# Kernel optimization log

Measured on AMD Instinct MI355X. Metric: run time of the kernel, lower is better.

The kernel has to match this reference:

```python
import jax, jax.numpy as jnp
import numpy as np
from jax import lax

B, L, H = 2, 1024, 1024
D = 2048          # intermediate_size
N = 16            # ssm state size
K = 4             # conv kernel
R = 64            # time_step_rank


def setup_inputs() -> dict:
    key = jax.random.key(0)
    ks = jax.random.split(key, 10)
    def nrm(k, shape, scale=0.02):
        return jax.random.normal(k, shape, dtype=jnp.float32) * scale
    A = jnp.arange(1, N + 1, dtype=jnp.float32)[None, :] * jnp.ones((D, 1), jnp.float32)
    return {
        "hidden_states": jax.random.normal(ks[0], (B, L, H), dtype=jnp.float32),
        "W_in":  nrm(ks[1], (2 * D, H)),
        "conv_w": nrm(ks[2], (D, 1, K), 0.1),
        "conv_b": nrm(ks[3], (D,), 0.1),
        "W_x":   nrm(ks[4], (R + 2 * N, D)),
        "W_dt":  nrm(ks[5], (D, R), 0.1),
        "b_dt":  jnp.full((D,), -4.6, jnp.float32),  # softplus(-4.6) ~ 0.01 dt init
        "A_log": jnp.log(A),
        "D_param": jnp.ones((D,), jnp.float32),
        "W_out": nrm(ks[6], (H, D)),
    }


def _mamba_forward(hidden_states, W_in, conv_w, conv_b, W_x, W_dt, b_dt, A_log, D_param, W_out):
    silu = jax.nn.silu
    # in_proj -> [B, L, 2D], chunk into x and gate
    proj = jnp.einsum("blh,eh->ble", hidden_states, W_in)
    x, gate = jnp.split(proj, 2, axis=-1)           # [B,L,D] each
    # depthwise causal conv over time: [B,D,L]
    xc = x.swapaxes(1, 2)
    xc = lax.conv_general_dilated(
        xc, conv_w, window_strides=(1,), padding=[(K - 1, 0)],
        dimension_numbers=("NCH", "OIH", "NCH"), feature_group_count=D)
    x = silu(xc + conv_b[None, :, None]).swapaxes(1, 2)   # [B,L,D]
    # x_proj -> dt, Bmat, Cmat
    ssm_p = jnp.einsum("bld,rd->blr", x, W_x)             # [B,L,R+2N]
    dt_lr, Bm, Cm = ssm_p[..., :R], ssm_p[..., R:R + N], ssm_p[..., R + N:]
    dt = jax.nn.softplus(jnp.einsum("blr,dr->bld", dt_lr, W_dt) + b_dt)  # [B,L,D]
    A = -jnp.exp(A_log)                                   # [D,N]
    dA = jnp.exp(dt[..., None] * A[None, None])           # [B,L,D,N]
    dBu = dt[..., None] * Bm[:, :, None, :] * x[..., None]  # [B,L,D,N]
    # selective scan over time
    def step(h, inp):
        dA_t, dBu_t, C_t = inp                            # [B,D,N],[B,D,N],[B,N]
        h = dA_t * h + dBu_t
        y = jnp.einsum("bdn,bn->bd", h, C_t)
        return h, y
    h0 = jnp.zeros((B, D, N), dt.dtype)
    _, ys = lax.scan(step, h0, (dA.swapaxes(0, 1), dBu.swapaxes(0, 1), Cm.swapaxes(0, 1)))
    y = ys.swapaxes(0, 1)                                 # [B,L,D]
    y = (y + x * D_param[None, None, :]) * silu(gate)
    return jnp.einsum("bld,hd->blh", y, W_out)            # [B,L,H]


def reference(hidden_states, W_in, conv_w, conv_b, W_x, W_dt, b_dt, A_log, D_param, W_out):
    return _mamba_forward(hidden_states, W_in, conv_w, conv_b, W_x, W_dt, b_dt, A_log, D_param, W_out)
```

## Files before the change

### kernel.cpp

```cpp
#include <hip/hip_runtime.h>
#include <hip/hip_bf16.h>
#include <math.h>

#define B_ 2
#define L_ 1024
#define H_ 1024
#define D_ 2048
#define N_ 16
#define R_ 64
#define NCK 32
#define CL 32

typedef short short8 __attribute__((ext_vector_type(8)));
typedef float floatx4 __attribute__((ext_vector_type(4)));

__device__ __forceinline__ float siluf(float g) {
    return g / (1.0f + __expf(-g));
}

__device__ __forceinline__ unsigned short f2bf(float f) {
    unsigned int u = __float_as_uint(f);
    u = (u + 0x7fffu + ((u >> 16) & 1u)) >> 16;
    return (unsigned short)u;
}

__device__ __forceinline__ float bf2f(unsigned short u) {
    return __uint_as_float(((unsigned int)u) << 16);
}

__device__ __forceinline__ void gl2lds(const unsigned short* g, unsigned short* l) {
    __builtin_amdgcn_global_load_lds(
        (const __attribute__((address_space(1))) unsigned int*)g,
        (__attribute__((address_space(3))) unsigned int*)l, 16, 0, 0);
}

#define Q0 524288
#define Q1 1572864
#define Q2 2097152
#define Q3 2146304
#define Q4 2179072
__global__ __launch_bounds__(256) void cvt_all(
    const float* __restrict__ i0, const float* __restrict__ i1,
    const float* __restrict__ i2, const float* __restrict__ i3,
    const float* __restrict__ i4,
    unsigned short* __restrict__ o0, unsigned short* __restrict__ o1,
    unsigned short* __restrict__ o2, unsigned short* __restrict__ o3,
    unsigned short* __restrict__ o4)
{
    int q = blockIdx.x * 256 + threadIdx.x;
    if (q >= Q4) return;
    const float* in; unsigned short* out; int base;
    if (q < Q0)      { in = i0; out = o0; base = 0; }
    else if (q < Q1) { in = i1; out = o1; base = Q0; }
    else if (q < Q2) { in = i2; out = o2; base = Q1; }
    else if (q < Q3) { in = i3; out = o3; base = Q2; }
    else             { in = i4; out = o4; base = Q3; }
    int i = (q - base) * 4;
    float4 v = *(const float4*)(in + i);
    ushort4 o;
    o.x = f2bf(v.x); o.y = f2bf(v.y); o.z = f2bf(v.z); o.w = f2bf(v.w);
    *(ushort4*)(out + i) = o;
}

template<int EPI>
__global__ __launch_bounds__(256) void gemm_bf16_nt(
    const unsigned short* __restrict__ A, const unsigned short* __restrict__ Bm,
    float* __restrict__ C, int K, int Ncols, int ldc, int kChunk, int nMax,
    size_t partStride, float* __restrict__ C2)
{
    __shared__ unsigned short As[2][64 * 64];
    __shared__ unsigned short Bs[2][128 * 64];
    const int tid  = threadIdx.x;
    const int lane = tid & 63;
    const int wave = tid >> 6;
    const int wm = (wave >> 1) * 32;
    const int wn = (wave & 1) * 64;
    const int lr   = lane & 15;
    const int quad = lane >> 4;
    const int m0 = blockIdx.y * 64;
    const int n0 = blockIdx.x * 128;
    const int k0 = blockIdx.z * kChunk;

    const int rowIn8 = lane >> 3;
    const int colSw  = ((lane & 7) ^ rowIn8) * 8;
    const size_t aoff0 = (size_t)(m0 + 0  + wave * 8 + rowIn8) * K + colSw;
    const size_t aoff1 = (size_t)(m0 + 32 + wave * 8 + rowIn8) * K + colSw;
    const size_t boff0 = (size_t)min(n0 + 0  + wave * 8 + rowIn8, nMax - 1) * K + colSw;
    const size_t boff1 = (size_t)min(n0 + 32 + wave * 8 + rowIn8, nMax - 1) * K + colSw;
    const size_t boff2 = (size_t)min(n0 + 64 + wave * 8 + rowIn8, nMax - 1) * K + colSw;
    const size_t boff3 = (size_t)min(n0 + 96 + wave * 8 + rowIn8, nMax - 1) * K + colSw;
    const int rq0 = ((quad) ^ (lr & 7)) * 8;
    const int rq1 = rq0 ^ 32;

    floatx4 acc[2][4];
#pragma unroll
    for (int mi = 0; mi < 2; ++mi)
#pragma unroll
        for (int ni = 0; ni < 4; ++ni)
            acc[mi][ni] = (floatx4){0.f, 0.f, 0.f, 0.f};

#define STAGE(buf, kt)                                                   \
    do {                                                                 \
        gl2lds(A + aoff0 + (kt), &As[buf][(0  + wave * 8) * 64]);        \
        gl2lds(A + aoff1 + (kt), &As[buf][(32 + wave * 8) * 64]);        \
        gl2lds(Bm + boff0 + (kt), &Bs[buf][(0   + wave * 8) * 64]);      \
        gl2lds(Bm + boff1 + (kt), &Bs[buf][(32  + wave * 8) * 64]);      \
        gl2lds(Bm + boff2 + (kt), &Bs[buf][(64  + wave * 8) * 64]);      \
        gl2lds(Bm + boff3 + (kt), &Bs[buf][(96  + wave * 8) * 64]);      \
    } while (0)

    STAGE(0, k0);

    const int nt = kChunk >> 6;
    for (int t = 0; t < nt; ++t) {
        const int cur = t & 1;
        if (t + 1 < nt) {
            STAGE(cur ^ 1, k0 + (t + 1) * 64);
            asm volatile("s_waitcnt vmcnt(6)" ::: "memory");
        } else {
            asm volatile("s_waitcnt vmcnt(0)" ::: "memory");
        }
        __builtin_amdgcn_s_barrier();
        __builtin_amdgcn_sched_barrier(0);

        short8 a0[2], a1[2], b0[4], b1[4];
#pragma unroll
        for (int mi = 0; mi < 2; ++mi) {
            a0[mi] = *(const short8*)&As[cur][(wm + mi * 16 + lr) * 64 + rq0];
            a1[mi] = *(const short8*)&As[cur][(wm + mi * 16 + lr) * 64 + rq1];
        }
#pragma unroll
        for (int ni = 0; ni < 4; ++ni) {
            b0[ni] = *(const short8*)&Bs[cur][(wn + ni * 16 + lr) * 64 + rq0];
            b1[ni] = *(const short8*)&Bs[cur][(wn + ni * 16 + lr) * 64 + rq1];
        }
#pragma unroll
        for (int mi = 0; mi < 2; ++mi)
#pragma unroll
            for (int ni = 0; ni < 4; ++ni)
                acc[mi][ni] = __builtin_amdgcn_mfma_f32_16x16x32_bf16(
                    a0[mi], b0[ni], acc[mi][ni], 0, 0, 0);
#pragma unroll
        for (int mi = 0; mi < 2; ++mi)
#pragma unroll
            for (int ni = 0; ni < 4; ++ni)
                acc[mi][ni] = __builtin_amdgcn_mfma_f32_16x16x32_bf16(
                    a1[mi], b1[ni], acc[mi][ni], 0, 0, 0);

        asm volatile("s_waitcnt lgkmcnt(0)" ::: "memory");
        __builtin_amdgcn_s_barrier();
    }
#undef STAGE

    float* Cz = C + (size_t)blockIdx.z * partStride;
#pragma unroll
    for (int mi = 0; mi < 2; ++mi)
#pragma unroll
        for (int ni = 0; ni < 4; ++ni) {
            const int rr = m0 + wm + mi * 16 + quad * 4;
            const int cc = n0 + wn + ni * 16 + lr;
            if (cc >= Ncols) continue;
            if (EPI == 4) {
                if (cc < 2048) {
#pragma unroll
                    for (int r = 0; r < 4; ++r)
                        C[(size_t)(rr + r) * 2048 + cc] = acc[mi][ni][r];
                } else {
#pragma unroll
                    for (int r = 0; r < 4; ++r)
                        C2[(size_t)(rr + r) * 2048 + (cc - 2048)] = acc[mi][ni][r];
                }
            } else {
#pragma unroll
                for (int r = 0; r < 4; ++r)
                    Cz[(size_t)(rr + r) * ldc + cc] = acc[mi][ni][r];
            }
        }
}

__global__ __launch_bounds__(256) void reduce_ssm(
    const float* __restrict__ P, float* __restrict__ ssm_p,
    unsigned short* __restrict__ sp64)
{
    const int q = blockIdx.x * 256 + threadIdx.x;
    const int m = q / 24;
    const int c = (q - m * 24) * 4;
    const size_t idx = (size_t)m * 96 + c;
    float4 s = make_float4(0.f, 0.f, 0.f, 0.f);
#pragma unroll
    for (int z = 0; z < 16; ++z) {
        float4 v = *(const float4*)(P + (size_t)z * (2048 * 96) + idx);
        s.x += v.x; s.y += v.y; s.z += v.z; s.w += v.w;
    }
    *(float4*)(ssm_p + idx) = s;
    if (c < 64) {
        ushort4 o;
        o.x = f2bf(s.x); o.y = f2bf(s.y); o.z = f2bf(s.z); o.w = f2bf(s.w);
        *(ushort4*)(sp64 + (size_t)m * 64 + c) = o;
    }
}

__global__ __launch_bounds__(256) void reduce_out(
    const float* __restrict__ P, float* __restrict__ out)
{
    const size_t i = ((size_t)blockIdx.x * 256 + threadIdx.x) * 4;
    float4 a = *(const float4*)(P + i);
    float4 b = *(const float4*)(P + 2097152 + i);
    *(float4*)(out + i) = make_float4(a.x + b.x, a.y + b.y, a.z + b.z, a.w + b.w);
}

__global__ __launch_bounds__(256) void dt_gemm(
    const unsigned short* __restrict__ A,
    const unsigned short* __restrict__ Bm,
    float* __restrict__ C,
    const float* __restrict__ bias)
{
    __shared__ unsigned short As[64 * 72];
    __shared__ unsigned short Bs[64 * 72];
    const int tid = threadIdx.x;
    const int lane = tid & 63;
    const int wave = tid >> 6;
    const int lr = lane & 15;
    const int quad = lane >> 4;
    const int n0 = blockIdx.x * 64;
    const int m0 = blockIdx.y * 64;

    {
        const int row = tid >> 3;
        const int cq = (tid & 7) * 8;
        uint4 a0 = *(const uint4*)(A + (size_t)(m0 + row) * 64 + cq);
        uint4 a1 = *(const uint4*)(A + (size_t)(m0 + 32 + row) * 64 + cq);
        uint4 b0 = *(const uint4*)(Bm + (size_t)(n0 + row) * 64 + cq);
        uint4 b1 = *(const uint4*)(Bm + (size_t)(n0 + 32 + row) * 64 + cq);
        *(uint4*)&As[row * 72 + cq] = a0;
        *(uint4*)&As[(32 + row) * 72 + cq] = a1;
        *(uint4*)&Bs[row * 72 + cq] = b0;
        *(uint4*)&Bs[(32 + row) * 72 + cq] = b1;
    }
    __syncthreads();

    floatx4 acc[4];
#pragma unroll
    for (int ni = 0; ni < 4; ++ni) acc[ni] = (floatx4){0.f, 0.f, 0.f, 0.f};

#pragma unroll
    for (int kt = 0; kt < 64; kt += 32) {
        short8 af = *(const short8*)&As[(wave * 16 + lr) * 72 + kt + quad * 8];
#pragma unroll
        for (int ni = 0; ni < 4; ++ni) {
            short8 bf = *(const short8*)&Bs[(ni * 16 + lr) * 72 + kt + quad * 8];
            acc[ni] = __builtin_amdgcn_mfma_f32_16x16x32_bf16(af, bf, acc[ni], 0, 0, 0);
        }
    }

    const int rr = m0 + wave * 16 + quad * 4;
#pragma unroll
    for (int ni = 0; ni < 4; ++ni) {
        const int cc = n0 + ni * 16 + lr;
        const float bv = bias[cc];
#pragma unroll
        for (int r = 0; r < 4; ++r) {
            const float z = acc[ni][r] + bv;
            const float spv = fmaxf(z, 0.f) + __logf(1.f + __expf(-fabsf(z)));
            C[(size_t)(rr + r) * 2048 + cc] = spv;
        }
    }
}

__global__ __launch_bounds__(256) void conv_silu_kernel(
    const float* __restrict__ xpre, const float* __restrict__ conv_w,
    const float* __restrict__ conv_b, unsigned short* __restrict__ x_bf)
{
    __shared__ float inT[67][64];
    __shared__ unsigned short tile[64][72];
    const int t = threadIdx.x;
    const int d0 = blockIdx.x * 64;
    const int lt0 = blockIdx.y * 64;
    const int b = blockIdx.z;

    {
        const int r = t >> 2;
        const int q = (t & 3) * 16;
        const int l = lt0 + r - 3;
        if (l >= 0) {
            const float* src = xpre + ((size_t)(b * 1024 + l)) * 2048 + d0 + q;
            *(float4*)&inT[r][q + 0]  = *(const float4*)(src + 0);
            *(float4*)&inT[r][q + 4]  = *(const float4*)(src + 4);
            *(float4*)&inT[r][q + 8]  = *(const float4*)(src + 8);
            *(float4*)&inT[r][q + 12] = *(const float4*)(src + 12);
        } else {
            float4 z4 = make_float4(0.f, 0.f, 0.f, 0.f);
            *(float4*)&inT[r][q + 0]  = z4;
            *(float4*)&inT[r][q + 4]  = z4;
            *(float4*)&inT[r][q + 8]  = z4;
            *(float4*)&inT[r][q + 12] = z4;
        }
        if (t < 12) {
            const int r2 = 64 + (t >> 2);
            const int l2 = lt0 + r2 - 3;
            const float* src = xpre + ((size_t)(b * 1024 + l2)) * 2048 + d0 + q;
            *(float4*)&inT[r2][q + 0]  = *(const float4*)(src + 0);
            *(float4*)&inT[r2][q + 4]  = *(const float4*)(src + 4);
            *(float4*)&inT[r2][q + 8]  = *(const float4*)(src + 8);
            *(float4*)&inT[r2][q + 12] = *(const float4*)(src + 12);
        }
    }
    __syncthreads();

    const int dl = t & 63;
    const int seg = t >> 6;
    const int d = d0 + dl;
    const float w0 = conv_w[d * 4 + 0], w1 = conv_w[d * 4 + 1];
    const float w2 = conv_w[d * 4 + 2], w3 = conv_w[d * 4 + 3];
    const float bias = conv_b[d];

    float p[19];
#pragma unroll
    for (int j = 0; j < 19; ++j) p[j] = inT[seg * 16 + j][dl];
#pragma unroll
    for (int j = 0; j < 16; ++j) {
        float v = siluf(bias + w0 * p[j] + w1 * p[j + 1] + w2 * p[j + 2] + w3 * p[j + 3]);
        tile[seg * 16 + j][dl] = f2bf(v);
    }
    __syncthreads();

    const int ml = t >> 2;
    const int c = t & 3;
    short8 s0 = *(const short8*)&tile[ml][c * 16];
    short8 s1 = *(const short8*)&tile[ml][c * 16 + 8];
    unsigned short* dst = x_bf + (size_t)(b * 1024 + lt0 + ml) * 2048 + d0 + c * 16;
    *(short8*)dst = s0;
    *(short8*)(dst + 8) = s1;
}

__global__ __launch_bounds__(256) void scan_p1(
    const float* __restrict__ dt, const unsigned short* __restrict__ x_bf,
    const float* __restrict__ sp, const float* __restrict__ A_log,
    float* __restrict__ Dts, float* __restrict__ Hch)
{
    __shared__ float sB[CL][16];
    const int tid = threadIdx.x;
    const int d = blockIdx.x * 256 + tid;
    const int ck = blockIdx.y;
    const int b = blockIdx.z;
    const int mb = b * 1024 + ck * CL;

    if (tid < CL * 4) {
        int row = tid >> 2, q = (tid & 3) * 4;
        *(float4*)&sB[row][q] = *(const float4*)(sp + (size_t)(mb + row) * 96 + 64 + q);
    }
    float An2[16];
    {
        const float* al = A_log + d * 16;
#pragma unroll
        for (int j = 0; j < 16; j += 4) {
            float4 a4 = *(const float4*)(al + j);
            An2[j + 0] = -__expf(a4.x) * 1.44269504f;
            An2[j + 1] = -__expf(a4.y) * 1.44269504f;
            An2[j + 2] = -__expf(a4.z) * 1.44269504f;
            An2[j + 3] = -__expf(a4.w) * 1.44269504f;
        }
    }
    __syncthreads();

    float h[16];
#pragma unroll
    for (int n = 0; n < 16; ++n) h[n] = 0.f;
    float dts = 0.f;

    for (int l = 0; l < CL; ++l) {
        const size_t off = (size_t)(mb + l) * 2048 + d;
        const float dtv = dt[off];
        const float xv = bf2f(x_bf[off]);
        const float u = dtv * xv;
        dts += dtv;
        float4 B0 = *(const float4*)&sB[l][0];
        float4 B1 = *(const float4*)&sB[l][4];
        float4 B2 = *(const float4*)&sB[l][8];
        float4 B3 = *(const float4*)&sB[l][12];
        float Bv[16] = {B0.x, B0.y, B0.z, B0.w, B1.x, B1.y, B1.z, B1.w,
                        B2.x, B2.y, B2.z, B2.w, B3.x, B3.y, B3.z, B3.w};
#pragma unroll
        for (int n = 0; n < 16; ++n) {
            const float dA = __builtin_amdgcn_exp2f(dtv * An2[n]);
            h[n] = fmaf(dA, h[n], Bv[n] * u);
        }
    }

    const size_t cb = (size_t)(b * NCK + ck) * 2048 + d;
    Dts[cb] = dts;
    const size_t base = cb * 16;
#pragma unroll
    for (int j = 0; j < 16; j += 4)
        *(float4*)(Hch + base + j) = make_float4(h[j], h[j + 1], h[j + 2], h[j + 3]);
}

__global__ __launch_bounds__(256) void scan_combine(
    const float* __restrict__ Dts, const float* __restrict__ Hch,
    const float* __restrict__ A_log, float* __restrict__ Hin)
{
    const int flat = blockIdx.x * 256 + threadIdx.x;
    const int dn = flat & 32767;
    const int b = flat >> 15;
    const int d = dn >> 4;
    const float An2 = -__expf(A_log[dn]) * 1.44269504f;
    float hin = 0.f;
#pragma unroll 4
    for (int ck = 0; ck < NCK; ++ck) {
        const size_t cb = (size_t)(b * NCK + ck) * 2048 + d;
        const float p = __builtin_amdgcn_exp2f(Dts[cb] * An2);
        const size_t a = ((size_t)(b * NCK + ck) << 15) + dn;
        const float hc = Hch[a];
        Hin[a] = hin;
        hin = fmaf(p, hin, hc);
    }
}

__global__ __launch_bounds__(256) void scan_p2(
    const float* __restrict__ dt, const unsigned short* __restrict__ x_bf,
    const float* __restrict__ gate, const float* __restrict__ sp,
    const float* __restrict__ A_log, const float* __restrict__ Dp,
    const float* __restrict__ Hin, unsigned short* __restrict__ y_bf)
{
    __shared__ float sBC[CL][32];
    const int tid = threadIdx.x;
    const int d = blockIdx.x * 256 + tid;
    const int ck = blockIdx.y;
    const int b = blockIdx.z;
    const int mb = b * 1024 + ck * CL;

    {
        int row = tid >> 3, q = (tid & 7) * 4;
        *(float4*)&sBC[row][q] = *(const float4*)(sp + (size_t)(mb + row) * 96 + 64 + q);
    }
    float An2[16];
    {
        const float* al = A_log + d * 16;
#pragma unroll
        for (int j = 0; j < 16; j += 4) {
            float4 a4 = *(const float4*)(al + j);
            An2[j + 0] = -__expf(a4.x) * 1.44269504f;
            An2[j + 1] = -__expf(a4.y) * 1.44269504f;
            An2[j + 2] = -__expf(a4.z) * 1.44269504f;
            An2[j + 3] = -__expf(a4.w) * 1.44269504f;
        }
    }
    float h[16];
    {
        const size_t base = ((size_t)(b * NCK + ck) * 2048 + d) * 16;
#pragma unroll
        for (int j = 0; j < 16; j += 4) {
            float4 hv = *(const float4*)(Hin + base + j);
            h[j] = hv.x; h[j + 1] = hv.y; h[j + 2] = hv.z; h[j + 3] = hv.w;
        }
    }
    const float Dv = Dp[d];
    __syncthreads();

    for (int l = 0; l < CL; ++l) {
        const size_t off = (size_t)(mb + l) * 2048 + d;
        const float dtv = dt[off];
        const float xv = bf2f(x_bf[off]);
        const float gv = gate[off];
        const float u = dtv * xv;
        float4 B0 = *(const float4*)&sBC[l][0];
        float4 B1 = *(const float4*)&sBC[l][4];
        float4 B2 = *(const float4*)&sBC[l][8];
        float4 B3 = *(const float4*)&sBC[l][12];
        float Bv[16] = {B0.x, B0.y, B0.z, B0.w, B1.x, B1.y, B1.z, B1.w,
                        B2.x, B2.y, B2.z, B2.w, B3.x, B3.y, B3.z, B3.w};
#pragma unroll
        for (int n = 0; n < 16; ++n) {
            const float dA = __builtin_amdgcn_exp2f(dtv * An2[n]);
            h[n] = fmaf(dA, h[n], Bv[n] * u);
        }
        float4 C0 = *(const float4*)&sBC[l][16];
        float4 C1 = *(const float4*)&sBC[l][20];
        float4 C2 = *(const float4*)&sBC[l][24];
        float4 C3 = *(const float4*)&sBC[l][28];
        float Cv[16] = {C0.x, C0.y, C0.z, C0.w, C1.x, C1.y, C1.z, C1.w,
                        C2.x, C2.y, C2.z, C2.w, C3.x, C3.y, C3.z, C3.w};
        float p = 0.f;
#pragma unroll
        for (int n = 0; n < 16; ++n)
            p = fmaf(h[n], Cv[n], p);
        y_bf[off] = f2bf(fmaf(xv, Dv, p) * siluf(gv));
    }
}

extern "C" void kernel_launch(void* const* d_in, const int* in_sizes, int n_in,
                              void* d_out, int out_size, void* d_ws, size_t ws_size,
                              hipStream_t stream)
{
    const float* hs     = (const float*)d_in[0];
    const float* W_in   = (const float*)d_in[1];
    const float* conv_w = (const float*)d_in[2];
    const float* conv_b = (const float*)d_in[3];
    const float* W_x    = (const float*)d_in[4];
    const float* W_dt   = (const float*)d_in[5];
    const float* b_dt   = (const float*)d_in[6];
    const float* A_log  = (const float*)d_in[7];
    const float* Dp     = (const float*)d_in[8];
    const float* W_out  = (const float*)d_in[9];
    float* out = (float*)d_out;

    float* ws    = (float*)d_ws;
    float* gate  = ws;
    float* dtb   = gate + (size_t)4194304;
    float* xpre  = dtb + (size_t)4194304;
    float* ssm_p = xpre + (size_t)4194304;
    unsigned short* hs_bf    = (unsigned short*)(ssm_p + 196608);
    unsigned short* W_in_bf  = hs_bf + (size_t)2097152;
    unsigned short* W_out_bf = W_in_bf + (size_t)4194304;
    unsigned short* W_x_bf   = W_out_bf + (size_t)2097152;
    unsigned short* W_dt_bf  = W_x_bf + (size_t)196608;
    unsigned short* sp64_bf  = W_dt_bf + (size_t)131072;
    unsigned short* x_bf     = sp64_bf + (size_t)131072;
    float* Dts  = (float*)(x_bf + (size_t)4194304);
    float* P1   = xpre;
    float* Hin  = xpre;
    float* Hch  = xpre + (size_t)2097152;
    float* Pout = gate;
    unsigned short* y_bf = hs_bf;

    const int M = B_ * L_;

    cvt_all<<<(Q4 + 255) / 256, 256, 0, stream>>>(
        hs, W_in, W_out, W_x, W_dt, hs_bf, W_in_bf, W_out_bf, W_x_bf, W_dt_bf);

    gemm_bf16_nt<4><<<dim3(4096 / 128, M / 64, 1), 256, 0, stream>>>(
        hs_bf, W_in_bf, xpre, 1024, 4096, 2048, 1024, 4096, 0, gate);

    conv_silu_kernel<<<dim3(D_ / 64, L_ / 64, B_), 256, 0, stream>>>(
        xpre, conv_w, conv_b, x_bf);

    gemm_bf16_nt<0><<<dim3(1, M / 64, 16), 256, 0, stream>>>(
        x_bf, W_x_bf, P1, 2048, 96, 96, 128, 96, (size_t)2048 * 96, nullptr);

    reduce_ssm<<<(2048 * 24) / 256, 256, 0, stream>>>(P1, ssm_p, sp64_bf);

    dt_gemm<<<dim3(2048 / 64, 2048 / 64), 256, 0, stream>>>(
        sp64_bf, W_dt_bf, dtb, b_dt);

    scan_p1<<<dim3(D_ / 256, NCK, B_), 256, 0, stream>>>(
        dtb, x_bf, ssm_p, A_log, Dts, Hch);
    scan_combine<<<(B_ * D_ * 16) / 256, 256, 0, stream>>>(Dts, Hch, A_log, Hin);
    scan_p2<<<dim3(D_ / 256, NCK, B_), 256, 0, stream>>>(
        dtb, x_bf, gate, ssm_p, A_log, Dp, Hin, y_bf);

    gemm_bf16_nt<0><<<dim3(1024 / 128, M / 64, 2), 256, 0, stream>>>(
        y_bf, W_out_bf, Pout, 2048, 1024, 1024, 1024, 1024, (size_t)2048 * 1024, nullptr);

    reduce_out<<<(2048 * 1024 / 4) / 256, 256, 0, stream>>>(Pout, out);
}
```

Baseline: 227.0 us.

## Use 128x128 tile GEMM for in/out projections with split-K 4 on out_proj

Adds a gemm128 kernel that computes 128x128 output tiles per block with a 4x4 MFMA accumulator grid per wave, replacing the 64x128 tiles for the in_proj and out_proj GEMMs. The larger tile is meant to raise data reuse from LDS and cut global loads per FLOP. The out_proj split-K factor rises from 2 to 4 (kChunk 512), and reduce_out now sums four partials. This doubles the partial buffer traffic and puts more pressure on registers, and the larger Pout footprint may go past the space reserved in the gate buffer. The old kernel is kept as gemm_ssm for the x_proj GEMM only.

```diff
diff --git a/kernel.cpp b/kernel.cpp
--- a/kernel.cpp
+++ b/kernel.cpp
@@ -63,10 +63,129 @@
 }
 
 template<int EPI>
-__global__ __launch_bounds__(256) void gemm_bf16_nt(
+__global__ __launch_bounds__(256) void gemm128(
+    const unsigned short* __restrict__ A, const unsigned short* __restrict__ Bm,
+    float* __restrict__ C, int K, int ldc, int kChunk,
+    size_t partStride, float* __restrict__ C2)
+{
+    __shared__ unsigned short As[2][128 * 64];
+    __shared__ unsigned short Bs[2][128 * 64];
+    const int tid  = threadIdx.x;
+    const int lane = tid & 63;
+    const int wave = tid >> 6;
+    const int wm = (wave >> 1) * 64;
+    const int wn = (wave & 1) * 64;
+    const int lr   = lane & 15;
+    const int quad = lane >> 4;
+    const int m0 = blockIdx.y * 128;
+    const int n0 = blockIdx.x * 128;
+    const int k0 = blockIdx.z * kChunk;
+
+    const int rowIn8 = lane >> 3;
+    const int colSw  = ((lane & 7) ^ rowIn8) * 8;
+    const int srow   = wave * 8 + rowIn8;
+    const size_t aoff0 = (size_t)(m0 + srow +  0) * K + colSw;
+    const size_t aoff1 = (size_t)(m0 + srow + 32) * K + colSw;
+    const size_t aoff2 = (size_t)(m0 + srow + 64) * K + colSw;
+    const size_t aoff3 = (size_t)(m0 + srow + 96) * K + colSw;
+    const size_t boff0 = (size_t)(n0 + srow +  0) * K + colSw;
+    const size_t boff1 = (size_t)(n0 + srow + 32) * K + colSw;
+    const size_t boff2 = (size_t)(n0 + srow + 64) * K + colSw;
+    const size_t boff3 = (size_t)(n0 + srow + 96) * K + colSw;
+    const int rq0 = ((quad) ^ (lr & 7)) * 8;
+    const int rq1 = rq0 ^ 32;
+
+    floatx4 acc[4][4];
+#pragma unroll
+    for (int mi = 0; mi < 4; ++mi)
+#pragma unroll
+        for (int ni = 0; ni < 4; ++ni)
+            acc[mi][ni] = (floatx4){0.f, 0.f, 0.f, 0.f};
+
+#define STG(buf, kt)                                                    \
+    do {                                                                \
+        gl2lds(A + aoff0 + (kt), &As[buf][(0  + wave * 8) * 64]);       \
+        gl2lds(A + aoff1 + (kt), &As[buf][(32 + wave * 8) * 64]);       \
+        gl2lds(A + aoff2 + (kt), &As[buf][(64 + wave * 8) * 64]);       \
+        gl2lds(A + aoff3 + (kt), &As[buf][(96 + wave * 8) * 64]);       \
+        gl2lds(Bm + boff0 + (kt), &Bs[buf][(0  + wave * 8) * 64]);      \
+        gl2lds(Bm + boff1 + (kt), &Bs[buf][(32 + wave * 8) * 64]);      \
+        gl2lds(Bm + boff2 + (kt), &Bs[buf][(64 + wave * 8) * 64]);      \
+        gl2lds(Bm + boff3 + (kt), &Bs[buf][(96 + wave * 8) * 64]);      \
+    } while (0)
+
+    STG(0, k0);
+
+    const int nt = kChunk >> 6;
+    for (int t = 0; t < nt; ++t) {
+        const int cur = t & 1;
+        if (t + 1 < nt) {
+            STG(cur ^ 1, k0 + (t + 1) * 64);
+            asm volatile("s_waitcnt vmcnt(8)" ::: "memory");
+        } else {
+            asm volatile("s_waitcnt vmcnt(0)" ::: "memory");
+        }
+        __builtin_amdgcn_s_barrier();
+        __builtin_amdgcn_sched_barrier(0);
+
+        short8 a0f[4], a1f[4], b0f[4], b1f[4];
+#pragma unroll
+        for (int mi = 0; mi < 4; ++mi) {
+            a0f[mi] = *(const short8*)&As[cur][(wm + mi * 16 + lr) * 64 + rq0];
+            a1f[mi] = *(const short8*)&As[cur][(wm + mi * 16 + lr) * 64 + rq1];
+        }
+#pragma unroll
+        for (int ni = 0; ni < 4; ++ni) {
+            b0f[ni] = *(const short8*)&Bs[cur][(wn + ni * 16 + lr) * 64 + rq0];
+            b1f[ni] = *(const short8*)&Bs[cur][(wn + ni * 16 + lr) * 64 + rq1];
+        }
+#pragma unroll
+        for (int mi = 0; mi < 4; ++mi)
+#pragma unroll
+            for (int ni = 0; ni < 4; ++ni)
+                acc[mi][ni] = __builtin_amdgcn_mfma_f32_16x16x32_bf16(
+                    a0f[mi], b0f[ni], acc[mi][ni], 0, 0, 0);
+#pragma unroll
+        for (int mi = 0; mi < 4; ++mi)
+#pragma unroll
+            for (int ni = 0; ni < 4; ++ni)
+                acc[mi][ni] = __builtin_amdgcn_mfma_f32_16x16x32_bf16(
+                    a1f[mi], b1f[ni], acc[mi][ni], 0, 0, 0);
+
+        asm volatile("s_waitcnt lgkmcnt(0)" ::: "memory");
+        __builtin_amdgcn_s_barrier();
+    }
+#undef STG
+
+    float* Cz = C + (size_t)blockIdx.z * partStride;
+#pragma unroll
+    for (int mi = 0; mi < 4; ++mi)
+#pragma unroll
+        for (int ni = 0; ni < 4; ++ni) {
+            const int rr = m0 + wm + mi * 16 + quad * 4;
+            const int cc = n0 + wn + ni * 16 + lr;
+            if (EPI == 4) {
+                if (cc < 2048) {
+#pragma unroll
+                    for (int r = 0; r < 4; ++r)
+                        C[(size_t)(rr + r) * 2048 + cc] = acc[mi][ni][r];
+                } else {
+#pragma unroll
+                    for (int r = 0; r < 4; ++r)
+                        C2[(size_t)(rr + r) * 2048 + (cc - 2048)] = acc[mi][ni][r];
+                }
+            } else {
+#pragma unroll
+                for (int r = 0; r < 4; ++r)
+                    Cz[(size_t)(rr + r) * ldc + cc] = acc[mi][ni][r];
+            }
+        }
+}
+
+__global__ __launch_bounds__(256) void gemm_ssm(
     const unsigned short* __restrict__ A, const unsigned short* __restrict__ Bm,
     float* __restrict__ C, int K, int Ncols, int ldc, int kChunk, int nMax,
-    size_t partStride, float* __restrict__ C2)
+    size_t partStride)
 {
     __shared__ unsigned short As[2][64 * 64];
     __shared__ unsigned short Bs[2][128 * 64];
@@ -160,21 +279,9 @@
             const int rr = m0 + wm + mi * 16 + quad * 4;
             const int cc = n0 + wn + ni * 16 + lr;
             if (cc >= Ncols) continue;
-            if (EPI == 4) {
-                if (cc < 2048) {
-#pragma unroll
-                    for (int r = 0; r < 4; ++r)
-                        C[(size_t)(rr + r) * 2048 + cc] = acc[mi][ni][r];
-                } else {
-#pragma unroll
-                    for (int r = 0; r < 4; ++r)
-                        C2[(size_t)(rr + r) * 2048 + (cc - 2048)] = acc[mi][ni][r];
-                }
-            } else {
-#pragma unroll
-                for (int r = 0; r < 4; ++r)
-                    Cz[(size_t)(rr + r) * ldc + cc] = acc[mi][ni][r];
-            }
+#pragma unroll
+            for (int r = 0; r < 4; ++r)
+                Cz[(size_t)(rr + r) * ldc + cc] = acc[mi][ni][r];
         }
 }
 
@@ -206,7 +313,12 @@
     const size_t i = ((size_t)blockIdx.x * 256 + threadIdx.x) * 4;
     float4 a = *(const float4*)(P + i);
     float4 b = *(const float4*)(P + 2097152 + i);
-    *(float4*)(out + i) = make_float4(a.x + b.x, a.y + b.y, a.z + b.z, a.w + b.w);
+    float4 c = *(const float4*)(P + 2 * 2097152 + i);
+    float4 d = *(const float4*)(P + 3 * 2097152 + i);
+    *(float4*)(out + i) = make_float4(a.x + b.x + c.x + d.x,
+                                      a.y + b.y + c.y + d.y,
+                                      a.z + b.z + c.z + d.z,
+                                      a.w + b.w + c.w + d.w);
 }
 
 __global__ __launch_bounds__(256) void dt_gemm(
@@ -528,14 +640,14 @@
     cvt_all<<<(Q4 + 255) / 256, 256, 0, stream>>>(
         hs, W_in, W_out, W_x, W_dt, hs_bf, W_in_bf, W_out_bf, W_x_bf, W_dt_bf);
 
-    gemm_bf16_nt<4><<<dim3(4096 / 128, M / 64, 1), 256, 0, stream>>>(
-        hs_bf, W_in_bf, xpre, 1024, 4096, 2048, 1024, 4096, 0, gate);
+    gemm128<4><<<dim3(4096 / 128, M / 128, 1), 256, 0, stream>>>(
+        hs_bf, W_in_bf, xpre, 1024, 2048, 1024, 0, gate);
 
     conv_silu_kernel<<<dim3(D_ / 64, L_ / 64, B_), 256, 0, stream>>>(
         xpre, conv_w, conv_b, x_bf);
 
-    gemm_bf16_nt<0><<<dim3(1, M / 64, 16), 256, 0, stream>>>(
-        x_bf, W_x_bf, P1, 2048, 96, 96, 128, 96, (size_t)2048 * 96, nullptr);
+    gemm_ssm<<<dim3(1, M / 64, 16), 256, 0, stream>>>(
+        x_bf, W_x_bf, P1, 2048, 96, 96, 128, 96, (size_t)2048 * 96);
 
     reduce_ssm<<<(2048 * 24) / 256, 256, 0, stream>>>(P1, ssm_p, sp64_bf);
 
@@ -548,8 +660,8 @@
     scan_p2<<<dim3(D_ / 256, NCK, B_), 256, 0, stream>>>(
         dtb, x_bf, gate, ssm_p, A_log, Dp, Hin, y_bf);
 
-    gemm_bf16_nt<0><<<dim3(1024 / 128, M / 64, 2), 256, 0, stream>>>(
-        y_bf, W_out_bf, Pout, 2048, 1024, 1024, 1024, 1024, (size_t)2048 * 1024, nullptr);
+    gemm128<0><<<dim3(1024 / 128, M / 128, 4), 256, 0, stream>>>(
+        y_bf, W_out_bf, Pout, 2048, 1024, 512, (size_t)2048 * 1024, nullptr);
 
     reduce_out<<<(2048 * 1024 / 4) / 256, 256, 0, stream>>>(Pout, out);
 }
```

Result: faster. 219.5 us (-3.3%).
